# Kernel optimization log

Hardware: AMD Instinct MI355X
Metric: run time of the kernel (lower is better)

Reference implementation:

```python
import jax, jax.numpy as jnp
import numpy as np

B, S, D, O, E, K = 4, 8192, 1024, 1024, 4, 2

def setup_inputs() -> dict:
    key = jax.random.key(0)
    k1, k2, k3, k4, k5 = jax.random.split(key, 5)
    x = jax.random.normal(k1, (B, S, D), dtype=jnp.float32)
    expert_weights = jax.random.uniform(k2, (B, S, K), dtype=jnp.float32)
    top_k_indices = jax.random.randint(k3, (B, S, K), 0, E).astype(jnp.int64)
    # per-expert linear params: nn.Linear(unified_dim, output_dim) for each expert
    W = jax.random.normal(k4, (E, D, O), dtype=jnp.float32) * (1.0 / np.sqrt(D))
    b = jax.random.normal(k5, (E, O), dtype=jnp.float32) * 0.01
    return {"x": x, "expert_weights": expert_weights, "top_k_indices": top_k_indices, "W": W, "b": b}

def reference(x, expert_weights, top_k_indices, W, b):
    # Dense compute of all experts, as the torch module does: [B,S,E,O]
    expert_outputs = jnp.einsum('bsd,edo->bseo', x, W) + b  # broadcast bias [E,O]
    # Gather top-k expert outputs per token: idx [B,S,K] -> [B,S,K,O]
    gathered = jnp.take_along_axis(expert_outputs, top_k_indices[..., None].astype(jnp.int32), axis=2)
    # Weighted combine over k
    output = jnp.sum(expert_weights[..., None] * gathered, axis=2)  # [B,S,O]
    return output
```

## Files before the change

kernel.cpp:

```cpp
#include <hip/hip_runtime.h>
#include <hip/hip_bf16.h>
#include <stdint.h>

#define M_TOK 32768
#define DIM   1024
#define ODIM  1024
#define NEXP  4
#define KTOT  4096
#define NBIN  16
#define MTILES 272
#define PERM_LEN (MTILES * 128)
#define GEMM_GRID (8 * 34 * 16)

typedef unsigned short u16;
typedef __bf16 bf16x8 __attribute__((ext_vector_type(8)));
typedef float  f32x4  __attribute__((ext_vector_type(4)));

__device__ inline u16 f2bf(float f) {
  union { float f; unsigned u; } v; v.f = f;
  unsigned u = v.u;
  unsigned r = u + 0x7FFFu + ((u >> 16) & 1u);
  return (u16)(r >> 16);
}

__device__ inline unsigned pack2(float lo, float hi) {
  return (unsigned)f2bf(lo) | ((unsigned)f2bf(hi) << 16);
}

__device__ inline void async16(const void* g, void* l) {
  __builtin_amdgcn_global_load_lds(
      (const __attribute__((address_space(1))) unsigned int*)g,
      (__attribute__((address_space(3))) unsigned int*)l, 16, 0, 0);
}

__global__ void cvt_x(const float4* __restrict__ x, uint4* __restrict__ xb, int n8) {
  int i = blockIdx.x * blockDim.x + threadIdx.x;
  int stride = gridDim.x * blockDim.x;
  for (; i < n8; i += stride) {
    float4 a = x[2 * i];
    float4 b = x[2 * i + 1];
    uint4 o;
    o.x = pack2(a.x, a.y); o.y = pack2(a.z, a.w);
    o.z = pack2(b.x, b.y); o.w = pack2(b.z, b.w);
    xb[i] = o;
  }
}

__global__ void cvt_wt(const float* __restrict__ W, u16* __restrict__ Wt) {
  __shared__ float t[32][33];
  int kk0 = blockIdx.x * 32, n0 = blockIdx.y * 32;
  int tx = threadIdx.x, ty = threadIdx.y;
#pragma unroll
  for (int j = 0; j < 32; j += 8)
    t[ty + j][tx] = W[(size_t)(kk0 + ty + j) * ODIM + n0 + tx];
  __syncthreads();
#pragma unroll
  for (int j = 0; j < 32; j += 8)
    Wt[(size_t)(n0 + ty + j) * KTOT + kk0 + tx] = f2bf(t[tx][ty + j]);
}

__global__ void init_ctrl(int* __restrict__ ctrl, int* __restrict__ perm) {
  int i = blockIdx.x * blockDim.x + threadIdx.x;
  if (i < 32) ctrl[i] = 0;
  for (int j = i; j < PERM_LEN; j += gridDim.x * blockDim.x) perm[j] = -1;
}

__global__ void hist(const int* __restrict__ tki, int* __restrict__ ctrl) {
  __shared__ int h[NBIN];
  int tid = threadIdx.x;
  if (tid < NBIN) h[tid] = 0;
  __syncthreads();
  int t = blockIdx.x * 256 + tid;
  int e0 = tki[2 * t] & 3, e1 = tki[2 * t + 1] & 3;
  atomicAdd(&h[e0 * 4 + e1], 1);
  __syncthreads();
  if (tid < NBIN) atomicAdd(&ctrl[tid], h[tid]);
}

__global__ void plan(int* __restrict__ ctrl) {
  if (threadIdx.x == 0 && blockIdx.x == 0) {
    int off = 0;
#pragma unroll
    for (int b = 0; b < NBIN; ++b) {
      ctrl[16 + b] = off;
      off += (ctrl[b] + 127) & ~127;
    }
  }
}

__global__ void scatter(const int* __restrict__ tki, const float* __restrict__ ew,
                        int* __restrict__ ctrl,
                        int* __restrict__ perm, float2* __restrict__ wgt2) {
  __shared__ int h[NBIN], gbase[NBIN], cur[NBIN];
  int tid = threadIdx.x;
  if (tid < NBIN) { h[tid] = 0; cur[tid] = 0; }
  __syncthreads();
  int t = blockIdx.x * 256 + tid;
  int e0 = tki[2 * t] & 3, e1 = tki[2 * t + 1] & 3;
  int bin = e0 * 4 + e1;
  atomicAdd(&h[bin], 1);
  __syncthreads();
  if (tid < NBIN && h[tid] > 0) gbase[tid] = atomicAdd(&ctrl[16 + tid], h[tid]);
  __syncthreads();
  int rank = atomicAdd(&cur[bin], 1);
  int pos = gbase[bin] + rank;
  perm[pos] = t;
  float2 w; w.x = ew[2 * t]; w.y = ew[2 * t + 1];
  wgt2[pos] = w;
}

__global__ __launch_bounds__(256, 4) void moe_gemm(
    const u16* __restrict__ Xb,
    const u16* __restrict__ Wt,
    const int* __restrict__ perm,
    const float2* __restrict__ wgt2,
    const int* __restrict__ tki,
    const float* __restrict__ bias,
    float* __restrict__ out)
{
  __shared__ __align__(16) u16 As [128 * 64];
  __shared__ __align__(16) u16 Bs0[64 * 64];
  __shared__ __align__(16) u16 Bs1[64 * 64];
  __shared__ int    rowsS[128];
  __shared__ float2 wgtS[128];

  const int d = blockIdx.x;
  const int slot = d >> 3;
  const int mtile = (d & 7) * (MTILES / 8) + (slot >> 4);
  const int nblk = slot & 15;
  const int base = mtile * 128;
  const int t0 = perm[base];
  if (t0 < 0) return;
  const int e0 = tki[2 * t0] & 3, e1 = tki[2 * t0 + 1] & 3;

  const int tid = threadIdx.x;
  if (tid < 128) { rowsS[tid] = perm[base + tid]; wgtS[tid] = wgt2[base + tid]; }

  const int wid = tid >> 6, lane = tid & 63;
  const int bcol = nblk * 64;
  const int wr = wid >> 1, wc = wid & 1;
  const int fcol = bcol + wc * 32;

  f32x4 acc0[4][2], acc1[4][2];
#pragma unroll
  for (int m = 0; m < 4; ++m)
#pragma unroll
    for (int n = 0; n < 2; ++n) {
      acc0[m][n] = (f32x4){0.f, 0.f, 0.f, 0.f};
      acc1[m][n] = (f32x4){0.f, 0.f, 0.f, 0.f};
    }

  const int srow = lane >> 3;
  const int scol = ((lane & 7) ^ srow) * 8;
  const int hi16 = (lane >> 4) * 16;
  const int swz  = (lane & 7) << 4;
  const char* AsB  = (const char*)As;
  const char* Bs0B = (const char*)Bs0;
  const char* Bs1B = (const char*)Bs1;

  __syncthreads();

  const u16* aptr[4];
  const u16* b0ptr[2];
  const u16* b1ptr[2];
#pragma unroll
  for (int i = 0; i < 4; ++i) {
    int c = wid * 4 + i;
    int r = rowsS[c * 8 + srow];
    if (r < 0) r = 0;
    aptr[i] = Xb + (size_t)r * DIM + scol;
  }
#pragma unroll
  for (int i = 0; i < 2; ++i) {
    int c = wid * 2 + i;
    size_t wrow = (size_t)(bcol + c * 8 + srow) * KTOT + scol;
    b0ptr[i] = Wt + wrow + e0 * DIM;
    b1ptr[i] = Wt + wrow + e1 * DIM;
  }

  for (int kt = 0; kt < DIM / 64; ++kt) {
    __syncthreads();
#pragma unroll
    for (int i = 0; i < 4; ++i)
      async16(aptr[i] + kt * 64, &As[(wid * 4 + i) * 512]);
#pragma unroll
    for (int i = 0; i < 2; ++i) {
      async16(b0ptr[i] + kt * 64, &Bs0[(wid * 2 + i) * 512]);
      async16(b1ptr[i] + kt * 64, &Bs1[(wid * 2 + i) * 512]);
    }
    __syncthreads();
#pragma unroll
    for (int kk = 0; kk < 2; ++kk) {
      const int cb = (kk * 64 + hi16) ^ swz;
      bf16x8 af[4], bf0[2], bf1[2];
#pragma unroll
      for (int m = 0; m < 4; ++m) {
        int row = wr * 64 + m * 16 + (lane & 15);
        af[m] = *reinterpret_cast<const bf16x8*>(AsB + row * 128 + cb);
      }
#pragma unroll
      for (int n = 0; n < 2; ++n) {
        int row = wc * 32 + n * 16 + (lane & 15);
        bf0[n] = *reinterpret_cast<const bf16x8*>(Bs0B + row * 128 + cb);
        bf1[n] = *reinterpret_cast<const bf16x8*>(Bs1B + row * 128 + cb);
      }
#pragma unroll
      for (int m = 0; m < 4; ++m)
#pragma unroll
        for (int n = 0; n < 2; ++n) {
          acc0[m][n] = __builtin_amdgcn_mfma_f32_16x16x32_bf16(af[m], bf0[n], acc0[m][n], 0, 0, 0);
          acc1[m][n] = __builtin_amdgcn_mfma_f32_16x16x32_bf16(af[m], bf1[n], acc1[m][n], 0, 0, 0);
        }
    }
  }

  float bb0[2], bb1[2];
#pragma unroll
  for (int n = 0; n < 2; ++n) {
    int col = fcol + n * 16 + (lane & 15);
    bb0[n] = bias[e0 * ODIM + col];
    bb1[n] = bias[e1 * ODIM + col];
  }

#pragma unroll
  for (int m = 0; m < 4; ++m) {
#pragma unroll
    for (int r = 0; r < 4; ++r) {
      int rl = wr * 64 + m * 16 + (lane >> 4) * 4 + r;
      int t = rowsS[rl];
      if (t < 0) continue;
      float2 w = wgtS[rl];
      size_t o = (size_t)t * ODIM + fcol + (lane & 15);
#pragma unroll
      for (int n = 0; n < 2; ++n)
        out[o + n * 16] = w.x * (acc0[m][n][r] + bb0[n]) + w.y * (acc1[m][n][r] + bb1[n]);
    }
  }
}

extern "C" void kernel_launch(void* const* d_in, const int* in_sizes, int n_in,
                              void* d_out, int out_size, void* d_ws, size_t ws_size,
                              hipStream_t stream) {
  const float* x    = (const float*)d_in[0];
  const float* ew   = (const float*)d_in[1];
  const int*   tki  = (const int*)d_in[2];
  const float* W    = (const float*)d_in[3];
  const float* bias = (const float*)d_in[4];
  float* out = (float*)d_out;

  char* ws = (char*)d_ws;
  u16*    xb   = (u16*)ws;
  u16*    wt   = (u16*)(ws + 67108864);
  int*    ctrl = (int*)(ws + 75497472);
  int*    perm = (int*)(ws + 75497728);
  float2* wgt2 = (float2*)(ws + 75636992);

  init_ctrl<<<64, 256, 0, stream>>>(ctrl, perm);
  cvt_x<<<4096, 256, 0, stream>>>((const float4*)x, (uint4*)xb, M_TOK * DIM / 8);
  cvt_wt<<<dim3(KTOT / 32, ODIM / 32), dim3(32, 8), 0, stream>>>(W, wt);
  hist<<<128, 256, 0, stream>>>(tki, ctrl);
  plan<<<1, 64, 0, stream>>>(ctrl);
  scatter<<<128, 256, 0, stream>>>(tki, ew, ctrl, perm, wgt2);
  moe_gemm<<<GEMM_GRID, 256, 0, stream>>>(xb, wt, perm, wgt2, tki, bias, out);
}
```

Baseline: 195.9 us.

## Enlarge GEMM M-tile to 256 rows with double-buffered async LDS pipeline

The grouped MoE GEMM now uses 256-row tiles and 512-thread blocks, with token bins padded to 256. Global-to-LDS loads are double-buffered and interleaved with four MFMA phases per k-step, using explicit barriers, waitcnt and setprio. The aim is to hide load latency and reuse each weight tile across more tokens. In exchange, a single block per CU and coarser padding mean more wasted rows and lower occupancy.

```diff
diff --git a/kernel.cpp b/kernel.cpp
--- a/kernel.cpp
+++ b/kernel.cpp
@@ -8,9 +8,12 @@
 #define NEXP  4
 #define KTOT  4096
 #define NBIN  16
-#define MTILES 272
-#define PERM_LEN (MTILES * 128)
-#define GEMM_GRID (8 * 34 * 16)
+#define BM    256
+#define BK    64
+#define NT    (DIM / BK)
+#define MTILES 144
+#define PERM_LEN (MTILES * 256)
+#define GEMM_GRID (MTILES * 16)
 
 typedef unsigned short u16;
 typedef __bf16 bf16x8 __attribute__((ext_vector_type(8)));
@@ -83,7 +86,7 @@
 #pragma unroll
     for (int b = 0; b < NBIN; ++b) {
       ctrl[16 + b] = off;
-      off += (ctrl[b] + 127) & ~127;
+      off += (ctrl[b] + 255) & ~255;
     }
   }
 }
@@ -109,7 +112,7 @@
   wgt2[pos] = w;
 }
 
-__global__ __launch_bounds__(256, 4) void moe_gemm(
+__global__ __launch_bounds__(512, 1) void moe_gemm(
     const u16* __restrict__ Xb,
     const u16* __restrict__ Wt,
     const int* __restrict__ perm,
@@ -118,23 +121,22 @@
     const float* __restrict__ bias,
     float* __restrict__ out)
 {
-  __shared__ __align__(16) u16 As [128 * 64];
-  __shared__ __align__(16) u16 Bs0[64 * 64];
-  __shared__ __align__(16) u16 Bs1[64 * 64];
-  __shared__ int    rowsS[128];
-  __shared__ float2 wgtS[128];
+  __shared__ __align__(16) u16 As[2][BM * BK];
+  __shared__ __align__(16) u16 Bs[2][2][64 * BK];
+  __shared__ int    rowsS[BM];
+  __shared__ float2 wgtS[BM];
 
   const int d = blockIdx.x;
   const int slot = d >> 3;
   const int mtile = (d & 7) * (MTILES / 8) + (slot >> 4);
   const int nblk = slot & 15;
-  const int base = mtile * 128;
+  const int base = mtile * BM;
   const int t0 = perm[base];
   if (t0 < 0) return;
   const int e0 = tki[2 * t0] & 3, e1 = tki[2 * t0 + 1] & 3;
 
   const int tid = threadIdx.x;
-  if (tid < 128) { rowsS[tid] = perm[base + tid]; wgtS[tid] = wgt2[base + tid]; }
+  if (tid < BM) { rowsS[tid] = perm[base + tid]; wgtS[tid] = wgt2[base + tid]; }
 
   const int wid = tid >> 6, lane = tid & 63;
   const int bcol = nblk * 64;
@@ -154,15 +156,10 @@
   const int scol = ((lane & 7) ^ srow) * 8;
   const int hi16 = (lane >> 4) * 16;
   const int swz  = (lane & 7) << 4;
-  const char* AsB  = (const char*)As;
-  const char* Bs0B = (const char*)Bs0;
-  const char* Bs1B = (const char*)Bs1;
 
   __syncthreads();
 
   const u16* aptr[4];
-  const u16* b0ptr[2];
-  const u16* b1ptr[2];
 #pragma unroll
   for (int i = 0; i < 4; ++i) {
     int c = wid * 4 + i;
@@ -170,48 +167,103 @@
     if (r < 0) r = 0;
     aptr[i] = Xb + (size_t)r * DIM + scol;
   }
-#pragma unroll
-  for (int i = 0; i < 2; ++i) {
-    int c = wid * 2 + i;
-    size_t wrow = (size_t)(bcol + c * 8 + srow) * KTOT + scol;
-    b0ptr[i] = Wt + wrow + e0 * DIM;
-    b1ptr[i] = Wt + wrow + e1 * DIM;
-  }
-
-  for (int kt = 0; kt < DIM / 64; ++kt) {
-    __syncthreads();
-#pragma unroll
-    for (int i = 0; i < 4; ++i)
-      async16(aptr[i] + kt * 64, &As[(wid * 4 + i) * 512]);
-#pragma unroll
-    for (int i = 0; i < 2; ++i) {
-      async16(b0ptr[i] + kt * 64, &Bs0[(wid * 2 + i) * 512]);
-      async16(b1ptr[i] + kt * 64, &Bs1[(wid * 2 + i) * 512]);
-    }
-    __syncthreads();
-#pragma unroll
-    for (int kk = 0; kk < 2; ++kk) {
-      const int cb = (kk * 64 + hi16) ^ swz;
-      bf16x8 af[4], bf0[2], bf1[2];
-#pragma unroll
-      for (int m = 0; m < 4; ++m) {
-        int row = wr * 64 + m * 16 + (lane & 15);
-        af[m] = *reinterpret_cast<const bf16x8*>(AsB + row * 128 + cb);
-      }
-#pragma unroll
-      for (int n = 0; n < 2; ++n) {
-        int row = wc * 32 + n * 16 + (lane & 15);
-        bf0[n] = *reinterpret_cast<const bf16x8*>(Bs0B + row * 128 + cb);
-        bf1[n] = *reinterpret_cast<const bf16x8*>(Bs1B + row * 128 + cb);
-      }
-#pragma unroll
-      for (int m = 0; m < 4; ++m)
-#pragma unroll
-        for (int n = 0; n < 2; ++n) {
-          acc0[m][n] = __builtin_amdgcn_mfma_f32_16x16x32_bf16(af[m], bf0[n], acc0[m][n], 0, 0, 0);
-          acc1[m][n] = __builtin_amdgcn_mfma_f32_16x16x32_bf16(af[m], bf1[n], acc1[m][n], 0, 0, 0);
-        }
-    }
+  const u16* b0ptr = Wt + (size_t)(bcol + wid * 8 + srow) * KTOT + e0 * DIM + scol;
+  const u16* b1ptr = Wt + (size_t)(bcol + wid * 8 + srow) * KTOT + e1 * DIM + scol;
+
+#define STAGE_AB0(bb, kt) do {                                          \
+    _Pragma("unroll")                                                   \
+    for (int i_ = 0; i_ < 4; ++i_)                                      \
+      async16(aptr[i_] + (kt) * 64, &As[bb][(wid * 4 + i_) * 512]);     \
+    async16(b0ptr + (kt) * 64, &Bs[bb][0][wid * 512]);                  \
+  } while (0)
+#define STAGE_B1(bb, kt) async16(b1ptr + (kt) * 64, &Bs[bb][1][wid * 512])
+#define SBAR() __builtin_amdgcn_s_barrier()
+#define LGKM0() do { asm volatile("s_waitcnt lgkmcnt(0)" ::: "memory"); \
+                     __builtin_amdgcn_sched_barrier(0); } while (0)
+
+  STAGE_AB0(0, 0);
+  STAGE_B1(0, 0);
+  STAGE_AB0(1, 1);
+  asm volatile("s_waitcnt vmcnt(5)" ::: "memory");
+  SBAR();
+
+  const int arow0 = wr * 64 + (lane & 15);
+  const int brow0 = wc * 32 + (lane & 15);
+
+  for (int kt = 0; kt < NT; ++kt) {
+    const int b = kt & 1;
+    const char* Ab  = (const char*)As[b];
+    const char* B0b = (const char*)Bs[b][0];
+    const char* B1b = (const char*)Bs[b][1];
+    const int cb0 = hi16 ^ swz;
+    const int cb1 = (64 + hi16) ^ swz;
+    bf16x8 af[4], bfr[2];
+
+#pragma unroll
+    for (int m = 0; m < 4; ++m)
+      af[m] = *reinterpret_cast<const bf16x8*>(Ab + (arow0 + m * 16) * 128 + cb0);
+#pragma unroll
+    for (int n = 0; n < 2; ++n)
+      bfr[n] = *reinterpret_cast<const bf16x8*>(B0b + (brow0 + n * 16) * 128 + cb0);
+    if (kt + 1 < NT) STAGE_B1(b ^ 1, kt + 1);
+    SBAR();
+    LGKM0();
+    __builtin_amdgcn_s_setprio(1);
+#pragma unroll
+    for (int m = 0; m < 4; ++m)
+#pragma unroll
+      for (int n = 0; n < 2; ++n)
+        acc0[m][n] = __builtin_amdgcn_mfma_f32_16x16x32_bf16(af[m], bfr[n], acc0[m][n], 0, 0, 0);
+    __builtin_amdgcn_s_setprio(0);
+    SBAR();
+
+#pragma unroll
+    for (int n = 0; n < 2; ++n)
+      bfr[n] = *reinterpret_cast<const bf16x8*>(B1b + (brow0 + n * 16) * 128 + cb0);
+    SBAR();
+    LGKM0();
+    __builtin_amdgcn_s_setprio(1);
+#pragma unroll
+    for (int m = 0; m < 4; ++m)
+#pragma unroll
+      for (int n = 0; n < 2; ++n)
+        acc1[m][n] = __builtin_amdgcn_mfma_f32_16x16x32_bf16(af[m], bfr[n], acc1[m][n], 0, 0, 0);
+    __builtin_amdgcn_s_setprio(0);
+    SBAR();
+
+#pragma unroll
+    for (int m = 0; m < 4; ++m)
+      af[m] = *reinterpret_cast<const bf16x8*>(Ab + (arow0 + m * 16) * 128 + cb1);
+#pragma unroll
+    for (int n = 0; n < 2; ++n)
+      bfr[n] = *reinterpret_cast<const bf16x8*>(B0b + (brow0 + n * 16) * 128 + cb1);
+    SBAR();
+    LGKM0();
+    __builtin_amdgcn_s_setprio(1);
+#pragma unroll
+    for (int m = 0; m < 4; ++m)
+#pragma unroll
+      for (int n = 0; n < 2; ++n)
+        acc0[m][n] = __builtin_amdgcn_mfma_f32_16x16x32_bf16(af[m], bfr[n], acc0[m][n], 0, 0, 0);
+    __builtin_amdgcn_s_setprio(0);
+    SBAR();
+
+#pragma unroll
+    for (int n = 0; n < 2; ++n)
+      bfr[n] = *reinterpret_cast<const bf16x8*>(B1b + (brow0 + n * 16) * 128 + cb1);
+    if (kt + 2 < NT) STAGE_AB0(b, kt + 2);
+    SBAR();
+    LGKM0();
+    __builtin_amdgcn_s_setprio(1);
+#pragma unroll
+    for (int m = 0; m < 4; ++m)
+#pragma unroll
+      for (int n = 0; n < 2; ++n)
+        acc1[m][n] = __builtin_amdgcn_mfma_f32_16x16x32_bf16(af[m], bfr[n], acc1[m][n], 0, 0, 0);
+    __builtin_amdgcn_s_setprio(0);
+    if (kt + 2 < NT) asm volatile("s_waitcnt vmcnt(5)" ::: "memory");
+    else             asm volatile("s_waitcnt vmcnt(0)" ::: "memory");
+    SBAR();
   }
 
   float bb0[2], bb1[2];
@@ -236,6 +288,10 @@
         out[o + n * 16] = w.x * (acc0[m][n][r] + bb0[n]) + w.y * (acc1[m][n][r] + bb1[n]);
     }
   }
+#undef STAGE_AB0
+#undef STAGE_B1
+#undef SBAR
+#undef LGKM0
 }
 
 extern "C" void kernel_launch(void* const* d_in, const int* in_sizes, int n_in,
@@ -253,7 +309,7 @@
   u16*    wt   = (u16*)(ws + 67108864);
   int*    ctrl = (int*)(ws + 75497472);
   int*    perm = (int*)(ws + 75497728);
-  float2* wgt2 = (float2*)(ws + 75636992);
+  float2* wgt2 = (float2*)(ws + 75645184);
 
   init_ctrl<<<64, 256, 0, stream>>>(ctrl, perm);
   cvt_x<<<4096, 256, 0, stream>>>((const float4*)x, (uint4*)xb, M_TOK * DIM / 8);
@@ -261,5 +317,5 @@
   hist<<<128, 256, 0, stream>>>(tki, ctrl);
   plan<<<1, 64, 0, stream>>>(ctrl);
   scatter<<<128, 256, 0, stream>>>(tki, ew, ctrl, perm, wgt2);
-  moe_gemm<<<GEMM_GRID, 256, 0, stream>>>(xb, wt, perm, wgt2, tki, bias, out);
-}
+  moe_gemm<<<GEMM_GRID, 512, 0, stream>>>(xb, wt, perm, wgt2, tki, bias, out);
+}
```

After: 283.6 us. 44.7% more time.
